# Performance work log

Hardware: AMD Instinct MI355X
Metric: run time of the kernel (lower is better)

## Reference

```python
import jax, jax.numpy as jnp
import numpy as np

B, L, HIDDEN = 64, 200, 256
HEADS = 8
MAX_WIDTH = 5
EPS = 1e-5  # F.layer_norm default eps


def _ln(x):
    # F.layer_norm with no learned affine
    m = jnp.mean(x, axis=-1, keepdims=True)
    v = jnp.mean((x - m) ** 2, axis=-1, keepdims=True)
    return (x - m) * jax.lax.rsqrt(v + EPS)


def _area_pool(x, max_width, mode):
    # x: [B, H, L, D] -> pooled spans of widths 1..max_width (valid windows),
    # concatenated along the memory axis: M = sum_w (L - w + 1)
    Lx = x.shape[2]
    outs = []
    for w in range(1, max_width + 1):
        # [w, B, H, L-w+1, D] stack of shifted slices (w <= 5, tiny loop)
        win = jnp.stack([x[:, :, i:Lx - w + 1 + i, :] for i in range(w)], axis=0)
        if mode == 'max':
            outs.append(win.max(axis=0))
        elif mode == 'mean':
            outs.append(win.mean(axis=0))
        else:  # 'sum'
            outs.append(win.sum(axis=0))
    return jnp.concatenate(outs, axis=2)


def _mha_area(q_in, k_in, v_in, Wq, bq, Wk, bk, Wv, bv, Wo, bo):
    # per-head size equals hidden_size (key_query_size_hidden = hidden_size)
    Bq, Lq, _ = q_in.shape
    Dh = Wq.shape[1] // HEADS

    def split(x):
        return x.reshape(x.shape[0], x.shape[1], HEADS, Dh).transpose(0, 2, 1, 3)

    q = split(q_in @ Wq + bq)  # [B, H, Lq, Dh]
    k = split(k_in @ Wk + bk)
    v = split(v_in @ Wv + bv)
    k_area = _area_pool(k, MAX_WIDTH, 'max')   # aggr='max' key pooling
    v_area = _area_pool(v, MAX_WIDTH, 'sum')   # values pooled by sum (t2t default)
    scale = jnp.asarray(1.0 / np.sqrt(Dh), q.dtype)
    logits = jnp.einsum('bhqd,bhmd->bhqm', q, k_area) * scale
    attn = jax.nn.softmax(logits, axis=-1)  # dropout inactive at eval
    out = jnp.einsum('bhqm,bhmd->bhqd', attn, v_area)
    out = out.transpose(0, 2, 1, 3).reshape(Bq, Lq, HEADS * Dh)
    return out @ Wo + bo


def setup_inputs() -> dict:
    key = jax.random.key(0)
    ks = jax.random.split(key, 16)
    stdv = 1.0 / np.sqrt(HIDDEN)
    u = lambda k, shp: jax.random.uniform(k, shp, jnp.float32, -stdv, stdv)
    HD = HEADS * HIDDEN  # 2048
    return {
        'A': jax.random.normal(ks[0], (B, L, L), jnp.float32),
        'hidden': jax.random.normal(ks[1], (B, L, HIDDEN), jnp.float32),
        'Wq': u(ks[2], (HIDDEN, HD)), 'bq': u(ks[3], (HD,)),
        'Wk': u(ks[4], (HIDDEN, HD)), 'bk': u(ks[5], (HD,)),
        'Wv': u(ks[6], (HIDDEN, HD)), 'bv': u(ks[7], (HD,)),
        'Wo': u(ks[8], (HD, HIDDEN)), 'bo': u(ks[9], (HIDDEN,)),
        'W1': u(ks[10], (HIDDEN, 4 * HIDDEN)), 'b1': u(ks[11], (4 * HIDDEN,)),
        'W2': u(ks[12], (4 * HIDDEN, HIDDEN)), 'b2': u(ks[13], (HIDDEN,)),
    }


def reference(A, hidden, Wq, bq, Wk, bk, Wv, bv, Wo, bo, W1, b1, W2, b2):
    # step = 1 -> single ATTNCell; A is unused by ATTNCell (matches source)
    attn1 = _mha_area(hidden, hidden, hidden, Wq, bq, Wk, bk, Wv, bv, Wo, bo)
    attn1 = _ln(attn1 + hidden)
    attn2 = _mha_area(attn1, hidden, hidden, Wq, bq, Wk, bk, Wv, bv, Wo, bo)
    attn2 = _ln(attn1 + attn2)  # F.dropout inactive (eval)
    x = jax.nn.relu(attn2 @ W1 + b1) @ W2 + b2
    return _ln(attn2 + x)
```

## Files before the change

kernel.cpp:

```cpp
#include <hip/hip_runtime.h>
#include <hip/hip_bf16.h>
#include <cstdint>
#include <cstddef>

#define BATCH 64
#define LSEQ 200
#define HID 256
#define NH 8
#define DH 256
#define HD (NH*DH)
#define MROWS (BATCH*LSEQ)
#define EPS 1e-5f
#define CSCALE 0.09014195f

typedef unsigned short ushort_t;
typedef __attribute__((ext_vector_type(8))) short bf16x8;
typedef __attribute__((ext_vector_type(8))) unsigned short u16x8;
typedef __attribute__((ext_vector_type(4))) float f32x4;

__device__ __forceinline__ float b2f(ushort_t u) {
    union { unsigned int i; float f; } c; c.i = ((unsigned int)u) << 16; return c.f;
}
__device__ __forceinline__ ushort_t f2b(float f) {
    __hip_bfloat16 h = __float2bfloat16(f);
    union { __hip_bfloat16 h; ushort_t u; } c; c.h = h; return c.u;
}
__device__ __forceinline__ ushort_t f2b_trunc(float f) {
    return (ushort_t)(__float_as_uint(f) >> 16);
}
__device__ __forceinline__ float to_f32(float x) { return x; }
__device__ __forceinline__ float to_f32(ushort_t x) { return b2f(x); }
__device__ __forceinline__ void store_val(float* p, float v) { *p = v; }
__device__ __forceinline__ void store_val(ushort_t* p, float v) { *p = f2b(v); }

__device__ __forceinline__ u16x8 bmax8(u16x8 a, u16x8 b) {
    union U { u16x8 v; __hip_bfloat162 h[4]; };
    U ua, ub, r; ua.v = a; ub.v = b;
    #pragma unroll
    for (int i = 0; i < 4; ++i) r.h[i] = __hmax2(ua.h[i], ub.h[i]);
    return r.v;
}
__device__ __forceinline__ u16x8 badd8(u16x8 a, u16x8 b) {
    union U { u16x8 v; __hip_bfloat162 h[4]; };
    U ua, ub, r; ua.v = a; ub.v = b;
    #pragma unroll
    for (int i = 0; i < 4; ++i) r.h[i] = __hadd2(ua.h[i], ub.h[i]);
    return r.v;
}

__device__ __forceinline__ void gll16(const void* g, void* l) {
    __builtin_amdgcn_global_load_lds(
        (const __attribute__((address_space(1))) unsigned int*)g,
        (__attribute__((address_space(3))) unsigned int*)l, 16, 0, 0);
}

template<bool RELU, int OMODE, bool SCALEC>
__global__ __launch_bounds__(256) void gemm_bt(
    const ushort_t* __restrict__ A, const ushort_t* __restrict__ Bt,
    const float* __restrict__ bias, ushort_t* __restrict__ C,
    int M, int N, int K)
{
    __shared__ ushort_t As[128 * 32];
    __shared__ ushort_t Bs[128 * 32];
    const int t = threadIdx.x;
    const int m0 = blockIdx.y * 128, n0 = blockIdx.x * 128;
    const int wave = t >> 6, lane = t & 63;
    const int l15 = lane & 15, lq = lane >> 4;
    const int wr = wave >> 1, wc = wave & 1;

    f32x4 acc[4][4];
    #pragma unroll
    for (int i = 0; i < 4; ++i)
        #pragma unroll
        for (int j = 0; j < 4; ++j) acc[i][j] = (f32x4){0.f, 0.f, 0.f, 0.f};

    for (int k0 = 0; k0 < K; k0 += 32) {
        __syncthreads();
        #pragma unroll
        for (int i = 0; i < 2; ++i) {
            int li = i * 256 + t;
            int ml = li >> 2, cp = li & 3;
            int cg = cp ^ ((ml ^ (ml >> 2)) & 3);
            gll16(A + (size_t)(m0 + ml) * K + k0 + cg * 8, &As[li * 8]);
        }
        #pragma unroll
        for (int i = 0; i < 2; ++i) {
            int li = i * 256 + t;
            int nl = li >> 2, cp = li & 3;
            int cg = cp ^ ((nl ^ (nl >> 2)) & 3);
            gll16(Bt + (size_t)(n0 + nl) * K + k0 + cg * 8, &Bs[li * 8]);
        }
        __syncthreads();
        bf16x8 af[4], bfr[4];
        #pragma unroll
        for (int i = 0; i < 4; ++i) {
            int r = wr * 64 + i * 16 + l15;
            int pc = lq ^ ((r ^ (r >> 2)) & 3);
            af[i] = *(const bf16x8*)&As[r * 32 + pc * 8];
        }
        #pragma unroll
        for (int j = 0; j < 4; ++j) {
            int r = wc * 64 + j * 16 + l15;
            int pc = lq ^ ((r ^ (r >> 2)) & 3);
            bfr[j] = *(const bf16x8*)&Bs[r * 32 + pc * 8];
        }
        #pragma unroll
        for (int i = 0; i < 4; ++i)
            #pragma unroll
            for (int j = 0; j < 4; ++j)
                acc[i][j] = __builtin_amdgcn_mfma_f32_16x16x32_bf16(af[i], bfr[j], acc[i][j], 0, 0, 0);
    }
    if (OMODE == 2) {
        #pragma unroll
        for (int i = 0; i < 4; ++i) {
            int mbase = m0 + wr * 64 + i * 16 + 4 * lq;
            int bb = (int)(((unsigned)mbase * 5243u) >> 20);
            int ll = mbase - bb * 200;
            #pragma unroll
            for (int j = 0; j < 4; ++j) {
                int n = n0 + wc * 64 + j * 16 + l15;
                float bsv = bias[n];
                ushort4 o4;
                o4.x = f2b(acc[i][j][0] + bsv); o4.y = f2b(acc[i][j][1] + bsv);
                o4.z = f2b(acc[i][j][2] + bsv); o4.w = f2b(acc[i][j][3] + bsv);
                size_t addr = ((size_t)(bb * NH + (n >> 8)) * 256 + (n & 255)) * LSEQ + ll;
                *(ushort4*)&C[addr] = o4;
            }
        }
    } else {
        #pragma unroll
        for (int i = 0; i < 4; ++i) {
            #pragma unroll
            for (int e = 0; e < 4; ++e) {
                int m = m0 + wr * 64 + i * 16 + 4 * lq + e;
                #pragma unroll
                for (int j = 0; j < 4; ++j) {
                    int n = n0 + wc * 64 + j * 16 + l15;
                    float v = acc[i][j][e] + bias[n];
                    if (RELU) v = fmaxf(v, 0.f);
                    if (SCALEC) v *= CSCALE;
                    if (OMODE == 1) {
                        int bb = (int)(((unsigned)m * 5243u) >> 20);
                        int ll = m - bb * 200;
                        size_t addr = ((((size_t)(bb * NH + (n >> 8))) * LSEQ + ll) << 8) + (n & 255);
                        C[addr] = f2b(v);
                    } else {
                        C[(size_t)m * N + n] = f2b(v);
                    }
                }
            }
        }
    }
}

__global__ __launch_bounds__(512, 2) void attn_mfma11(
    const ushort_t* __restrict__ Q, const ushort_t* __restrict__ Khm,
    const ushort_t* __restrict__ Vt, ushort_t* __restrict__ O)
{
    const int id = blockIdx.x;
    const int xcd = id & 7, slot_ = id >> 3;
    const int qt = slot_ & 1;
    const int bh = ((slot_ >> 1) << 3) + xcd;
    const int b = bh >> 3, h = bh & 7;
    const int q0 = qt * 128;
    const int t = threadIdx.x;
    const int wave = t >> 6, lane = t & 63;
    const int l15 = lane & 15, lq = lane >> 4;

    __shared__ ushort_t Ks[64 * 256];
    __shared__ ushort_t Vs[256 * 64];
    __shared__ ushort_t Ps[8][16][72];

    const ushort_t* kbh = Khm + (size_t)bh * LSEQ * DH;
    const ushort_t* vtb = Vt + (size_t)bh * DH * LSEQ;
    const ushort_t* qbh = Q + ((size_t)b * LSEQ) * HD + h * DH;
    const int qrow = q0 + wave * 16 + l15;

    bf16x8 qf[8];
    if (qrow < LSEQ) {
        const ushort_t* qp = qbh + (size_t)qrow * HD + 8 * lq;
        #pragma unroll
        for (int g = 0; g < 8; ++g) qf[g] = *(const bf16x8*)(qp + 32 * g);
    } else {
        bf16x8 zf = {0,0,0,0,0,0,0,0};
        #pragma unroll
        for (int g = 0; g < 8; ++g) qf[g] = zf;
    }

    f32x4 oacc[16];
    #pragma unroll
    for (int i = 0; i < 16; ++i) oacc[i] = (f32x4){0.f, 0.f, 0.f, 0.f};
    float l_st[4];
    #pragma unroll
    for (int e = 0; e < 4; ++e) l_st[e] = 0.f;

    const int dc = t & 31, mb = t >> 5;
    const int vd = t >> 1, vh = t & 1;

    auto step = [&](bool tail) {
        f32x4 sacc[4];
        #pragma unroll
        for (int ms = 0; ms < 4; ++ms) {
            f32x4 s = (f32x4){0.f, 0.f, 0.f, 0.f};
            const int row = ms * 16 + l15;
            #pragma unroll
            for (int g = 0; g < 8; ++g) {
                const int phys = (lq + 4 * g) ^ l15;
                s = __builtin_amdgcn_mfma_f32_16x16x32_bf16(
                        qf[g], *(const bf16x8*)&Ks[row * 256 + phys * 8], s, 0, 0, 0);
            }
            sacc[ms] = s;
        }
        if (tail) {
            #pragma unroll
            for (int ms = 0; ms < 4; ++ms) {
                const int slot = ms * 16 + l15;
                const bool inval = ((slot & 7) > 7 - (slot >> 3)) || ((slot >> 3) > 4);
                #pragma unroll
                for (int e = 0; e < 4; ++e)
                    if (inval) sacc[ms][e] = -1e30f;
            }
        }
        #pragma unroll
        for (int ms = 0; ms < 4; ++ms)
            #pragma unroll
            for (int e = 0; e < 4; ++e) {
                float pj = __builtin_exp2f(sacc[ms][e]);
                l_st[e] += pj;
                Ps[wave][4 * lq + e][ms * 16 + l15] = f2b_trunc(pj);
            }

        bf16x8 pf0 = *(const bf16x8*)&Ps[wave][l15][8 * lq];
        bf16x8 pf1 = *(const bf16x8*)&Ps[wave][l15][32 + 8 * lq];
        #pragma unroll
        for (int dt = 0; dt < 16; ++dt) {
            const int d = dt * 16 + l15;
            const int p0 = lq ^ (d & 7);
            const int p1 = (lq + 4) ^ (d & 7);
            oacc[dt] = __builtin_amdgcn_mfma_f32_16x16x32_bf16(
                           pf0, *(const bf16x8*)&Vs[d * 64 + p0 * 8], oacc[dt], 0, 0, 0);
            oacc[dt] = __builtin_amdgcn_mfma_f32_16x16x32_bf16(
                           pf1, *(const bf16x8*)&Vs[d * 64 + p1 * 8], oacc[dt], 0, 0, 0);
        }
    };

    for (int ti = 0; ti < 3; ++ti) {
        const int st0 = ti * 64;
        #pragma unroll
        for (int cls = 0; cls < 5; ++cls) {
            u16x8 kf[4];
            #pragma unroll
            for (int k4 = 0; k4 < 4; ++k4)
                kf[k4] = *(const u16x8*)(kbh + (size_t)(st0 + mb + 16 * k4 + cls) * DH + dc * 8);
            __syncthreads();

            #pragma unroll
            for (int k4 = 0; k4 < 4; ++k4) {
                int m = mb + 16 * k4;
                ushort_t* kp = &Ks[m * 256 + ((dc ^ (m & 15)) * 8)];
                *(u16x8*)kp = (cls == 0) ? kf[k4] : bmax8(*(const u16x8*)kp, kf[k4]);
            }
            {
                const ushort_t* vrow = vtb + (size_t)vd * LSEQ + st0 + vh * 32;
                u16x8 vc[5];
                #pragma unroll
                for (int c = 0; c < 5; ++c) vc[c] = *(const u16x8*)(vrow + c * 8);
                #pragma unroll
                for (int cl = 0; cl < 4; ++cl) {
                    const int cg = vh * 4 + cl;
                    ushort_t* vp = &Vs[vd * 64 + ((cg ^ (vd & 7)) * 8)];
                    if (cls == 0) {
                        *(u16x8*)vp = vc[cl];
                    } else {
                        u16x8 sh;
                        #pragma unroll
                        for (int j = 0; j < 8; ++j)
                            sh[j] = (j + cls < 8) ? vc[cl][j + cls] : vc[cl + 1][j + cls - 8];
                        *(u16x8*)vp = badd8(*(const u16x8*)vp, sh);
                    }
                }
            }
            __syncthreads();
            step(false);
        }
    }

    {
        __syncthreads();
        if (mb < 8) {
            u16x8 krun = *(const u16x8*)(kbh + (size_t)(192 + mb) * DH + dc * 8);
            const u16x8 kz = {0,0,0,0,0,0,0,0};
            #pragma unroll
            for (int k8 = 0; k8 < 8; ++k8) {
                const bool v = (k8 <= 4) && (mb <= 7 - k8);
                if (k8 > 0 && v)
                    krun = bmax8(krun, *(const u16x8*)(kbh + (size_t)(192 + mb + k8) * DH + dc * 8));
                int slot = k8 * 8 + mb;
                *(u16x8*)&Ks[slot * 256 + ((dc ^ (slot & 15)) * 8)] = v ? krun : kz;
            }
        }
        {
            u16x8 v0 = *(const u16x8*)(vtb + (size_t)vd * LSEQ + 192);
            float f[8], s[8];
            #pragma unroll
            for (int e = 0; e < 8; ++e) { f[e] = b2f(v0[e]); s[e] = f[e]; }
            #pragma unroll
            for (int cl = 0; cl < 4; ++cl) {
                const int c = vh * 4 + cl;
                u16x8 ov = {0,0,0,0,0,0,0,0};
                if (c <= 4) {
                    #pragma unroll
                    for (int u = 1; u <= 4; ++u)
                        if (u <= c)
                            #pragma unroll
                            for (int off = 0; off < 8; ++off)
                                if (off <= 7 - u && u == c)
                                    ;
                    #pragma unroll
                    for (int j = 0; j < 8; ++j) {
                        if (j <= 7 - c) {
                            float acc = 0.f;
                            #pragma unroll
                            for (int u = 0; u <= 4; ++u)
                                if (u <= c) acc += f[j + u];
                            ov[j] = f2b(acc);
                        }
                    }
                }
                *(u16x8*)&Vs[vd * 64 + ((c ^ (vd & 7)) * 8)] = ov;
            }
        }
        __syncthreads();
        step(true);
    }

    #pragma unroll
    for (int off = 1; off < 16; off <<= 1)
        #pragma unroll
        for (int e = 0; e < 4; ++e) l_st[e] += __shfl_xor(l_st[e], off);

    ushort_t* ob = O + ((size_t)b * LSEQ) * HD + h * DH;
    #pragma unroll
    for (int e = 0; e < 4; ++e) {
        const int q = q0 + wave * 16 + 4 * lq + e;
        if (q < LSEQ) {
            const float linv = 1.f / l_st[e];
            #pragma unroll
            for (int dt = 0; dt < 16; ++dt)
                ob[(size_t)q * HD + dt * 16 + l15] = f2b(oacc[dt][e] * linv);
        }
    }
}

template<typename TR, typename TO>
__global__ __launch_bounds__(256) void residual_ln(
    const ushort_t* __restrict__ X, const TR* __restrict__ R, TO* __restrict__ Out)
{
    const int row = blockIdx.x;
    const int t = threadIdx.x;
    const size_t base = (size_t)row * HID;
    float v = b2f(X[base + t]) + to_f32(R[base + t]);
    float s = v, q = v * v;
    #pragma unroll
    for (int o = 32; o > 0; o >>= 1) {
        s += __shfl_xor(s, o, 64);
        q += __shfl_xor(q, o, 64);
    }
    __shared__ float ss[4], sq[4];
    const int wave = t >> 6, lane = t & 63;
    if (lane == 0) { ss[wave] = s; sq[wave] = q; }
    __syncthreads();
    s = ss[0] + ss[1] + ss[2] + ss[3];
    q = sq[0] + sq[1] + sq[2] + sq[3];
    float mean = s * (1.f / HID);
    float var  = q * (1.f / HID) - mean * mean;
    store_val(&Out[base + t], (v - mean) * rsqrtf(var + EPS));
}

__global__ __launch_bounds__(256) void cvt_f32_bf16(const float* __restrict__ in,
                                                    ushort_t* __restrict__ out) {
    const int i = (blockIdx.x * 256 + threadIdx.x) * 4;
    float4 v = *(const float4*)(in + i);
    ushort4 o;
    o.x = f2b(v.x); o.y = f2b(v.y); o.z = f2b(v.z); o.w = f2b(v.w);
    *(ushort4*)(out + i) = o;
}

__global__ __launch_bounds__(256) void wtrans(const float* __restrict__ W,
                                              ushort_t* __restrict__ Wt, int K, int N) {
    __shared__ float tile[32][33];
    const int t = threadIdx.x;
    const int tx = t & 31, ty = t >> 5;
    const int n0 = blockIdx.x * 32, k0 = blockIdx.y * 32;
    #pragma unroll
    for (int s = 0; s < 4; ++s)
        tile[ty + 8 * s][tx] = W[(size_t)(k0 + ty + 8 * s) * N + n0 + tx];
    __syncthreads();
    #pragma unroll
    for (int s = 0; s < 4; ++s)
        Wt[(size_t)(n0 + ty + 8 * s) * K + k0 + tx] = f2b(tile[tx][ty + 8 * s]);
}

extern "C" void kernel_launch(void* const* d_in, const int* in_sizes, int n_in,
                              void* d_out, int out_size, void* d_ws, size_t ws_size,
                              hipStream_t stream) {
    const float* hidden = (const float*)d_in[1];
    const float* Wq = (const float*)d_in[2];  const float* bq = (const float*)d_in[3];
    const float* Wk = (const float*)d_in[4];  const float* bk = (const float*)d_in[5];
    const float* Wv = (const float*)d_in[6];  const float* bv = (const float*)d_in[7];
    const float* Wo = (const float*)d_in[8];  const float* bo = (const float*)d_in[9];
    const float* W1 = (const float*)d_in[10]; const float* b1 = (const float*)d_in[11];
    const float* W2 = (const float*)d_in[12]; const float* b2 = (const float*)d_in[13];
    float* out = (float*)d_out;

    constexpr size_t SZ_BF   = (size_t)MROWS * HD * 2;
    constexpr size_t SZ_HBF  = (size_t)MROWS * HID * 2;
    constexpr size_t SZ_WQKV = (size_t)HID * HD * 2;
    constexpr size_t SZ_W12  = (size_t)HID * 4 * HID * 2;
    char* ws = (char*)d_ws;
    size_t off = 0;
    ushort_t* kb   = (ushort_t*)(ws + off); off += SZ_BF;
    ushort_t* vt   = (ushort_t*)(ws + off); off += SZ_BF;
    ushort_t* qo   = (ushort_t*)(ws + off); off += SZ_BF;
    ushort_t* hb   = (ushort_t*)(ws + off); off += SZ_HBF;
    ushort_t* at1  = (ushort_t*)(ws + off); off += SZ_HBF;
    ushort_t* at2  = (ushort_t*)(ws + off); off += SZ_HBF;
    ushort_t* proj = (ushort_t*)(ws + off); off += SZ_HBF;
    ushort_t* WtQ  = (ushort_t*)(ws + off); off += SZ_WQKV;
    ushort_t* WtK  = (ushort_t*)(ws + off); off += SZ_WQKV;
    ushort_t* WtV  = (ushort_t*)(ws + off); off += SZ_WQKV;
    ushort_t* WtO  = (ushort_t*)(ws + off); off += SZ_WQKV;
    ushort_t* Wt1  = (ushort_t*)(ws + off); off += SZ_W12;
    ushort_t* Wt2  = (ushort_t*)(ws + off); off += SZ_W12;
    if (ws_size < off) return;
    ushort_t* ffn1 = qo;

    dim3 blk(256);
    cvt_f32_bf16<<<MROWS * HID / 1024, blk, 0, stream>>>(hidden, hb);
    wtrans<<<dim3(HD / 32, HID / 32), blk, 0, stream>>>(Wq, WtQ, HID, HD);
    wtrans<<<dim3(HD / 32, HID / 32), blk, 0, stream>>>(Wk, WtK, HID, HD);
    wtrans<<<dim3(HD / 32, HID / 32), blk, 0, stream>>>(Wv, WtV, HID, HD);
    wtrans<<<dim3(HID / 32, HD / 32), blk, 0, stream>>>(Wo, WtO, HD, HID);
    wtrans<<<dim3(4 * HID / 32, HID / 32), blk, 0, stream>>>(W1, Wt1, HID, 4 * HID);
    wtrans<<<dim3(HID / 32, 4 * HID / 32), blk, 0, stream>>>(W2, Wt2, 4 * HID, HID);

    const dim3 gProj(HD / 128, MROWS / 128);
    const dim3 gOut(HID / 128, MROWS / 128);
    const dim3 gF1(4 * HID / 128, MROWS / 128);

    gemm_bt<false, 1, false><<<gProj, blk, 0, stream>>>(hb, WtK, bk, kb, MROWS, HD, HID);
    gemm_bt<false, 2, false><<<gProj, blk, 0, stream>>>(hb, WtV, bv, vt, MROWS, HD, HID);

    gemm_bt<false, 0, true><<<gProj, blk, 0, stream>>>(hb, WtQ, bq, qo, MROWS, HD, HID);
    attn_mfma11<<<2 * BATCH * NH, 512, 0, stream>>>(qo, kb, vt, qo);
    gemm_bt<false, 0, false><<<gOut, blk, 0, stream>>>(qo, WtO, bo, proj, MROWS, HID, HD);
    residual_ln<float, ushort_t><<<MROWS, blk, 0, stream>>>(proj, hidden, at1);

    gemm_bt<false, 0, true><<<gProj, blk, 0, stream>>>(at1, WtQ, bq, qo, MROWS, HD, HID);
    attn_mfma11<<<2 * BATCH * NH, 512, 0, stream>>>(qo, kb, vt, qo);
    gemm_bt<false, 0, false><<<gOut, blk, 0, stream>>>(qo, WtO, bo, proj, MROWS, HID, HD);
    residual_ln<ushort_t, ushort_t><<<MROWS, blk, 0, stream>>>(proj, at1, at2);

    gemm_bt<true, 0, false><<<gF1, blk, 0, stream>>>(at2, Wt1, b1, ffn1, MROWS, 4 * HID, HID);
    gemm_bt<false, 0, false><<<gOut, blk, 0, stream>>>(ffn1, Wt2, b2, proj, MROWS, HID, 4 * HID);
    residual_ln<ushort_t, float><<<MROWS, blk, 0, stream>>>(proj, at2, out);
}
```

Measured before the change: 986.6 us.

## Keep softmax probabilities in registers by transposing QK MFMA and permuting V layout

The QK^T MFMA swaps its operands so each lane's score accumulator already matches the A-operand layout needed for the PV MFMA. This removes the per-wave LDS round trip through the Ps buffer. The V tile in LDS is stored with a permuted half-chunk layout to match the new register order of the probabilities. Probabilities are packed with v_cvt_pk_bf16_f32, the row-sum reduction is simplified, s_setprio brackets the MFMA phases, and launch bounds request 4 blocks per CU, which may raise register pressure or cause spills.

```diff
diff --git a/kernel.cpp b/kernel.cpp
--- a/kernel.cpp
+++ b/kernel.cpp
@@ -24,9 +24,6 @@
 __device__ __forceinline__ ushort_t f2b(float f) {
     __hip_bfloat16 h = __float2bfloat16(f);
     union { __hip_bfloat16 h; ushort_t u; } c; c.h = h; return c.u;
-}
-__device__ __forceinline__ ushort_t f2b_trunc(float f) {
-    return (ushort_t)(__float_as_uint(f) >> 16);
 }
 __device__ __forceinline__ float to_f32(float x) { return x; }
 __device__ __forceinline__ float to_f32(ushort_t x) { return b2f(x); }
@@ -153,7 +150,7 @@
     }
 }
 
-__global__ __launch_bounds__(512, 2) void attn_mfma11(
+__global__ __launch_bounds__(512, 4) void attn_mfma12(
     const ushort_t* __restrict__ Q, const ushort_t* __restrict__ Khm,
     const ushort_t* __restrict__ Vt, ushort_t* __restrict__ O)
 {
@@ -169,7 +166,6 @@
 
     __shared__ ushort_t Ks[64 * 256];
     __shared__ ushort_t Vs[256 * 64];
-    __shared__ ushort_t Ps[8][16][72];
 
     const ushort_t* kbh = Khm + (size_t)bh * LSEQ * DH;
     const ushort_t* vtb = Vt + (size_t)bh * DH * LSEQ;
@@ -190,15 +186,14 @@
     f32x4 oacc[16];
     #pragma unroll
     for (int i = 0; i < 16; ++i) oacc[i] = (f32x4){0.f, 0.f, 0.f, 0.f};
-    float l_st[4];
-    #pragma unroll
-    for (int e = 0; e < 4; ++e) l_st[e] = 0.f;
+    float l_part = 0.f;
 
     const int dc = t & 31, mb = t >> 5;
     const int vd = t >> 1, vh = t & 1;
 
     auto step = [&](bool tail) {
         f32x4 sacc[4];
+        __builtin_amdgcn_s_setprio(1);
         #pragma unroll
         for (int ms = 0; ms < 4; ++ms) {
             f32x4 s = (f32x4){0.f, 0.f, 0.f, 0.f};
@@ -207,31 +202,35 @@
             for (int g = 0; g < 8; ++g) {
                 const int phys = (lq + 4 * g) ^ l15;
                 s = __builtin_amdgcn_mfma_f32_16x16x32_bf16(
-                        qf[g], *(const bf16x8*)&Ks[row * 256 + phys * 8], s, 0, 0, 0);
+                        *(const bf16x8*)&Ks[row * 256 + phys * 8], qf[g], s, 0, 0, 0);
             }
             sacc[ms] = s;
         }
-        if (tail) {
-            #pragma unroll
-            for (int ms = 0; ms < 4; ++ms) {
-                const int slot = ms * 16 + l15;
-                const bool inval = ((slot & 7) > 7 - (slot >> 3)) || ((slot >> 3) > 4);
-                #pragma unroll
-                for (int e = 0; e < 4; ++e)
-                    if (inval) sacc[ms][e] = -1e30f;
-            }
-        }
-        #pragma unroll
-        for (int ms = 0; ms < 4; ++ms)
+        __builtin_amdgcn_s_setprio(0);
+        unsigned int w[8];
+        #pragma unroll
+        for (int ms = 0; ms < 4; ++ms) {
+            float pj[4];
             #pragma unroll
             for (int e = 0; e < 4; ++e) {
-                float pj = __builtin_exp2f(sacc[ms][e]);
-                l_st[e] += pj;
-                Ps[wave][4 * lq + e][ms * 16 + l15] = f2b_trunc(pj);
-            }
-
-        bf16x8 pf0 = *(const bf16x8*)&Ps[wave][l15][8 * lq];
-        bf16x8 pf1 = *(const bf16x8*)&Ps[wave][l15][32 + 8 * lq];
+                float sv = sacc[ms][e];
+                if (tail) {
+                    const int slot = ms * 16 + 4 * lq + e;
+                    if (((slot & 7) > 7 - (slot >> 3)) || ((slot >> 3) > 4)) sv = -1e30f;
+                }
+                float p = __builtin_exp2f(sv);
+                l_part += p;
+                pj[e] = p;
+            }
+            asm("v_cvt_pk_bf16_f32 %0, %1, %2" : "=v"(w[2*ms])   : "v"(pj[0]), "v"(pj[1]));
+            asm("v_cvt_pk_bf16_f32 %0, %1, %2" : "=v"(w[2*ms+1]) : "v"(pj[2]), "v"(pj[3]));
+        }
+        union FR { unsigned int u[4]; bf16x8 v; };
+        FR f0, f1;
+        f0.u[0] = w[0]; f0.u[1] = w[1]; f0.u[2] = w[2]; f0.u[3] = w[3];
+        f1.u[0] = w[4]; f1.u[1] = w[5]; f1.u[2] = w[6]; f1.u[3] = w[7];
+        const bf16x8 pf0 = f0.v, pf1 = f1.v;
+        __builtin_amdgcn_s_setprio(1);
         #pragma unroll
         for (int dt = 0; dt < 16; ++dt) {
             const int d = dt * 16 + l15;
@@ -242,6 +241,7 @@
             oacc[dt] = __builtin_amdgcn_mfma_f32_16x16x32_bf16(
                            pf1, *(const bf16x8*)&Vs[d * 64 + p1 * 8], oacc[dt], 0, 0, 0);
         }
+        __builtin_amdgcn_s_setprio(0);
     };
 
     for (int ti = 0; ti < 3; ++ti) {
@@ -268,16 +268,26 @@
                 #pragma unroll
                 for (int cl = 0; cl < 4; ++cl) {
                     const int cg = vh * 4 + cl;
-                    ushort_t* vp = &Vs[vd * 64 + ((cg ^ (vd & 7)) * 8)];
+                    const int kc = (cg >> 2) * 4 + (cg & 1) * 2;
+                    const int par4 = ((cg >> 1) & 1) * 4;
+                    ushort_t* plo = &Vs[vd * 64 + ((kc ^ (vd & 7)) * 8) + par4];
+                    ushort_t* phi = &Vs[vd * 64 + (((kc + 1) ^ (vd & 7)) * 8) + par4];
+                    union VH { u16x8 v; ushort4 h[2]; };
+                    VH nv;
                     if (cls == 0) {
-                        *(u16x8*)vp = vc[cl];
+                        nv.v = vc[cl];
                     } else {
                         u16x8 sh;
                         #pragma unroll
                         for (int j = 0; j < 8; ++j)
                             sh[j] = (j + cls < 8) ? vc[cl][j + cls] : vc[cl + 1][j + cls - 8];
-                        *(u16x8*)vp = badd8(*(const u16x8*)vp, sh);
+                        VH cur;
+                        cur.h[0] = *(const ushort4*)plo;
+                        cur.h[1] = *(const ushort4*)phi;
+                        nv.v = badd8(cur.v, sh);
                     }
+                    *(ushort4*)plo = nv.h[0];
+                    *(ushort4*)phi = nv.h[1];
                 }
             }
             __syncthreads();
@@ -301,21 +311,16 @@
         }
         {
             u16x8 v0 = *(const u16x8*)(vtb + (size_t)vd * LSEQ + 192);
-            float f[8], s[8];
-            #pragma unroll
-            for (int e = 0; e < 8; ++e) { f[e] = b2f(v0[e]); s[e] = f[e]; }
+            float f[8];
+            #pragma unroll
+            for (int e = 0; e < 8; ++e) f[e] = b2f(v0[e]);
             #pragma unroll
             for (int cl = 0; cl < 4; ++cl) {
                 const int c = vh * 4 + cl;
-                u16x8 ov = {0,0,0,0,0,0,0,0};
+                union VH { u16x8 v; ushort4 h[2]; } ov;
+                #pragma unroll
+                for (int j = 0; j < 8; ++j) ov.v[j] = 0;
                 if (c <= 4) {
-                    #pragma unroll
-                    for (int u = 1; u <= 4; ++u)
-                        if (u <= c)
-                            #pragma unroll
-                            for (int off = 0; off < 8; ++off)
-                                if (off <= 7 - u && u == c)
-                                    ;
                     #pragma unroll
                     for (int j = 0; j < 8; ++j) {
                         if (j <= 7 - c) {
@@ -323,28 +328,30 @@
                             #pragma unroll
                             for (int u = 0; u <= 4; ++u)
                                 if (u <= c) acc += f[j + u];
-                            ov[j] = f2b(acc);
+                            ov.v[j] = f2b(acc);
                         }
                     }
                 }
-                *(u16x8*)&Vs[vd * 64 + ((c ^ (vd & 7)) * 8)] = ov;
+                const int kc = (c >> 2) * 4 + (c & 1) * 2;
+                const int par4 = ((c >> 1) & 1) * 4;
+                *(ushort4*)&Vs[vd * 64 + ((kc ^ (vd & 7)) * 8) + par4] = ov.h[0];
+                *(ushort4*)&Vs[vd * 64 + (((kc + 1) ^ (vd & 7)) * 8) + par4] = ov.h[1];
             }
         }
         __syncthreads();
         step(true);
     }
 
-    #pragma unroll
-    for (int off = 1; off < 16; off <<= 1)
-        #pragma unroll
-        for (int e = 0; e < 4; ++e) l_st[e] += __shfl_xor(l_st[e], off);
+    l_part += __shfl_xor(l_part, 16);
+    l_part += __shfl_xor(l_part, 32);
+    const float inv = 1.f / l_part;
 
     ushort_t* ob = O + ((size_t)b * LSEQ) * HD + h * DH;
     #pragma unroll
     for (int e = 0; e < 4; ++e) {
         const int q = q0 + wave * 16 + 4 * lq + e;
+        const float linv = __shfl(inv, 4 * lq + e);
         if (q < LSEQ) {
-            const float linv = 1.f / l_st[e];
             #pragma unroll
             for (int dt = 0; dt < 16; ++dt)
                 ob[(size_t)q * HD + dt * 16 + l15] = f2b(oacc[dt][e] * linv);
@@ -452,12 +459,12 @@
     gemm_bt<false, 2, false><<<gProj, blk, 0, stream>>>(hb, WtV, bv, vt, MROWS, HD, HID);
 
     gemm_bt<false, 0, true><<<gProj, blk, 0, stream>>>(hb, WtQ, bq, qo, MROWS, HD, HID);
-    attn_mfma11<<<2 * BATCH * NH, 512, 0, stream>>>(qo, kb, vt, qo);
+    attn_mfma12<<<2 * BATCH * NH, 512, 0, stream>>>(qo, kb, vt, qo);
     gemm_bt<false, 0, false><<<gOut, blk, 0, stream>>>(qo, WtO, bo, proj, MROWS, HID, HD);
     residual_ln<float, ushort_t><<<MROWS, blk, 0, stream>>>(proj, hidden, at1);
 
     gemm_bt<false, 0, true><<<gProj, blk, 0, stream>>>(at1, WtQ, bq, qo, MROWS, HD, HID);
-    attn_mfma11<<<2 * BATCH * NH, 512, 0, stream>>>(qo, kb, vt, qo);
+    attn_mfma12<<<2 * BATCH * NH, 512, 0, stream>>>(qo, kb, vt, qo);
     gemm_bt<false, 0, false><<<gOut, blk, 0, stream>>>(qo, WtO, bo, proj, MROWS, HID, HD);
     residual_ln<ushort_t, ushort_t><<<MROWS, blk, 0, stream>>>(proj, at1, at2);
 
```

Measured after the change: 1.708 ms. +73.1%, slower.
